# Kernel tuning notes

Measured on AMD Instinct MI355X. Metric: run time of the kernel, lower is better.

## Reference

```python
import jax, jax.numpy as jnp
import numpy as np

N = 300000   # total nodes
C = 32       # hidden states
M = 64       # discrete label alphabet
NGEN = 8     # number of generative models
G = 8192     # number of graphs


def setup_inputs() -> dict:
    key = jax.random.key(0)
    k1, k2, k3, k4 = jax.random.split(key, 4)
    B = jax.random.uniform(k1, (C, M, NGEN), minval=-5.0, maxval=5.0, dtype=jnp.float32)
    Pi = jax.random.uniform(k2, (C, NGEN), minval=-5.0, maxval=5.0, dtype=jnp.float32)
    x = jax.random.randint(k3, (N,), 0, M)
    batch = jnp.sort(jax.random.randint(k4, (N,), 0, G))
    return {"B": B, "Pi": Pi, "x": x, "batch": batch, "num_graphs": G}


def reference(B, Pi, x, batch, num_graphs):
    # softmax reparameterization: over M for B, over C for Pi (per generator)
    sm_B = jax.nn.softmax(B, axis=1)          # (C, M, n_gen)
    sm_Pi = jax.nn.softmax(Pi, axis=0)        # (C, n_gen)
    # gather per-node emission probs, then joint with prior -> (N, C, n_gen)
    numerator = sm_Pi[None, :, :] * jnp.transpose(sm_B[:, x, :], (1, 0, 2))
    posterior = numerator / numerator.sum(axis=1, keepdims=True)  # (N, C, n_gen)
    likelihood = (posterior * jnp.log(numerator)).sum(axis=1)     # (N, n_gen)
    # scatter-sum per graph
    likelihood = jax.ops.segment_sum(likelihood, batch, num_segments=num_graphs)  # (G, n_gen)
    h_vals = posterior.max(axis=1, keepdims=True)   # (N, 1, n_gen)
    h_idx = posterior.argmax(axis=1)                # (N, n_gen)
    return likelihood, h_vals, h_idx
```

## Files before the change

kernel.cpp:

```cpp
#include <hip/hip_runtime.h>

#define C_DIM 32
#define M_DIM 64
#define NG    8
#define TAB   (M_DIM * NG)
#define ST    9
#define SPB   1024


__global__ void __launch_bounds__(256)
cgmm_partials(const float* __restrict__ B, const float* __restrict__ Pi,
              const int* __restrict__ batch,
              float* __restrict__ Sexp, float* __restrict__ lsePi,
              int* __restrict__ starts, int N, int G) {
    const int tid = threadIdx.x;
    const int bid = blockIdx.x;

    if (bid < C_DIM) {
        __shared__ float row_s[M_DIM * NG];
        const float* row = B + bid * (M_DIM * NG);
        row_s[tid]       = row[tid];
        row_s[tid + 256] = row[tid + 256];
        __syncthreads();
        if (tid < NG) {
            float s = 0.f;
            #pragma unroll
            for (int m = 0; m < M_DIM; ++m) s += __expf(row_s[m * NG + tid]);
            Sexp[bid * NG + tid] = s;
        }
        return;
    }
    if (bid == C_DIM) {
        __shared__ float pi_s[C_DIM * NG];
        pi_s[tid] = Pi[tid];
        __syncthreads();
        if (tid < NG) {
            float s = 0.f;
            #pragma unroll
            for (int c = 0; c < C_DIM; ++c) s += __expf(pi_s[c * NG + tid]);
            lsePi[tid] = __logf(s);
        }
        return;
    }

    const int base = (bid - C_DIM - 1) * SPB;
    for (int i = tid; i < SPB; i += 256) {
        const int n = base + i;
        if (n >= N) break;
        const int bn = batch[n];
        if (n == 0) {
            for (int j = 0; j <= bn; ++j) starts[j] = 0;
        } else {
            const int bp = batch[n - 1];
            for (int j = bp + 1; j <= bn; ++j) starts[j] = n;
        }
        if (n == N - 1) {
            for (int j = bn + 1; j <= G; ++j) starts[j] = N;
        }
    }
}

__global__ void __launch_bounds__(512)
cgmm_tables(const float* __restrict__ B, const float* __restrict__ Pi,
            const float* __restrict__ Sexp, const float* __restrict__ lsePi,
            float* __restrict__ tab) {
    __shared__ float K_s[C_DIM * NG];
    const int tid = threadIdx.x;
    if (tid < C_DIM * NG)
        K_s[tid] = Pi[tid] - __logf(Sexp[tid]) - lsePi[tid & 7];
    __syncthreads();

    const int g = tid & 7;
    float L[C_DIM];
    float best = -1e30f; int bidx = 0;
    #pragma unroll
    for (int c = 0; c < C_DIM; ++c) {
        float v = B[c * (M_DIM * NG) + tid] + K_s[c * NG + g];
        L[c] = v;
        if (v > best) { best = v; bidx = c; }
    }
    float se = 0.f, la = 0.f;
    #pragma unroll
    for (int c = 0; c < C_DIM; ++c) {
        float e = __expf(L[c] - best);
        se += e; la += e * L[c];
    }
    tab[tid]           = la / se;
    tab[TAB + tid]     = 1.f / se;
    tab[2 * TAB + tid] = (float)bidx;
}

__global__ void __launch_bounds__(512)
cgmm_write(const int* __restrict__ x, const int* __restrict__ starts,
           const float* __restrict__ tab,
           float* __restrict__ out_like, float* __restrict__ out_hv,
           float* __restrict__ out_hi, int G) {
    __shared__ float like_s[M_DIM * ST];
    __shared__ float hval_s[M_DIM * ST];
    __shared__ float hidx_s[M_DIM * ST];
    const int tid = threadIdx.x;
    for (int i = tid; i < TAB; i += 512) {
        const int p = (i >> 3) * ST + (i & 7);
        like_s[p] = tab[i];
        hval_s[p] = tab[TAB + i];
        hidx_s[p] = tab[2 * TAB + i];
    }
    __syncthreads();

    const int j = blockIdx.x * 8 + (tid >> 6);
    if (j >= G) return;
    const int start = starts[j];
    const int end   = starts[j + 1];

    const int lane = tid & 63;
    const int slot = lane >> 3;
    const int g    = lane & 7;

    float4* hv4 = (float4*)out_hv;
    float4* hi4 = (float4*)out_hi;

    float acc = 0.f;
    for (int cb = start; cb < end; cb += 64) {
        const int cnt = end - cb;
        const int xv  = (cb + lane < end) ? x[cb + lane] : 0;

        #pragma unroll
        for (int s = 0; s < 2; ++s) {
            const int f    = s * 64 + lane;
            const int node = f >> 1;
            const int h    = (f & 1) * 4;
            const int xm   = __shfl(xv, node);
            if (node < cnt) {
                const int p = xm * ST + h;
                float4 v, w;
                v.x = hval_s[p];     v.y = hval_s[p + 1];
                v.z = hval_s[p + 2]; v.w = hval_s[p + 3];
                w.x = hidx_s[p];     w.y = hidx_s[p + 1];
                w.z = hidx_s[p + 2]; w.w = hidx_s[p + 3];
                hv4[(size_t)cb * 2 + f] = v;
                hi4[(size_t)cb * 2 + f] = w;
            }
        }
        #pragma unroll
        for (int t = 0; t < 8; ++t) {
            const int node = slot + 8 * t;
            const int xm   = __shfl(xv, node);
            if (node < cnt) acc += like_s[xm * ST + g];
        }
    }
    acc += __shfl_xor(acc, 8);
    acc += __shfl_xor(acc, 16);
    acc += __shfl_xor(acc, 32);
    if (lane < NG) out_like[(size_t)j * NG + g] = acc;
}

extern "C" void kernel_launch(void* const* d_in, const int* in_sizes, int n_in,
                              void* d_out, int out_size, void* d_ws, size_t ws_size,
                              hipStream_t stream) {
    const float* B     = (const float*)d_in[0];
    const float* Pi    = (const float*)d_in[1];
    const int*   x     = (const int*)d_in[2];
    const int*   batch = (const int*)d_in[3];
    const int N = in_sizes[2];
    const int G = (out_size - 2 * N * NG) / NG;

    float* tab    = (float*)d_ws;
    float* Sexp   = (float*)((char*)d_ws + 8192);
    float* lsePi  = (float*)((char*)d_ws + 9216);
    int*   starts = (int*)((char*)d_ws + 16384);

    float* out_like = (float*)d_out;
    float* out_hv   = out_like + (size_t)G * NG;
    float* out_hi   = out_hv + (size_t)N * NG;

    const int nsb = (N + SPB - 1) / SPB;

    cgmm_partials<<<C_DIM + 1 + nsb, 256, 0, stream>>>(B, Pi, batch, Sexp,
                                                       lsePi, starts, N, G);
    cgmm_tables<<<1, 512, 0, stream>>>(B, Pi, Sexp, lsePi, tab);
    cgmm_write<<<(G + 7) / 8, 512, 0, stream>>>(x, starts, tab, out_like,
                                                out_hv, out_hi, G);
}
```

Measured before the change: 19.74 us.

## Fuse softmax-normalizer and table kernels into the prep kernel

Merges the partials and table-building kernels into one prep kernel. Eight blocks each load all of B and Pi into padded shared memory, recompute the per-row normalizers and the prior log-sum-exp redundantly, then each builds the table entries for 8 labels. This removes one kernel launch and its serialization, plus the global round trip for Sexp and lsePi. The cost is redundant normalizer work in every table block and a 64KB shared-memory footprint per block.

```diff
diff --git a/kernel.cpp b/kernel.cpp
--- a/kernel.cpp
+++ b/kernel.cpp
@@ -5,45 +5,77 @@
 #define NG    8
 #define TAB   (M_DIM * NG)
 #define ST    9
+#define BST   520
 #define SPB   1024
+#define NTB   8
 
 
 __global__ void __launch_bounds__(256)
-cgmm_partials(const float* __restrict__ B, const float* __restrict__ Pi,
-              const int* __restrict__ batch,
-              float* __restrict__ Sexp, float* __restrict__ lsePi,
-              int* __restrict__ starts, int N, int G) {
+cgmm_prep(const float* __restrict__ B, const float* __restrict__ Pi,
+          const int* __restrict__ batch,
+          float* __restrict__ tab, int* __restrict__ starts,
+          int N, int G) {
     const int tid = threadIdx.x;
     const int bid = blockIdx.x;
 
-    if (bid < C_DIM) {
-        __shared__ float row_s[M_DIM * NG];
-        const float* row = B + bid * (M_DIM * NG);
-        row_s[tid]       = row[tid];
-        row_s[tid + 256] = row[tid + 256];
+    if (bid < NTB) {
+        __shared__ float Bs[C_DIM * BST];
+        __shared__ float Pis[C_DIM * NG];
+        __shared__ float lsePi_s[NG];
+        __shared__ float K_s[C_DIM * NG];
+
+        const float4* B4 = (const float4*)B;
+        float4* Bs4 = (float4*)Bs;
+        #pragma unroll
+        for (int i = tid; i < (C_DIM * M_DIM * NG) / 4; i += 256)
+            Bs4[(i >> 7) * (BST / 4) + (i & 127)] = B4[i];
+        if (tid < C_DIM * NG / 4) ((float4*)Pis)[tid] = ((const float4*)Pi)[tid];
         __syncthreads();
+
         if (tid < NG) {
             float s = 0.f;
             #pragma unroll
-            for (int m = 0; m < M_DIM; ++m) s += __expf(row_s[m * NG + tid]);
-            Sexp[bid * NG + tid] = s;
+            for (int c = 0; c < C_DIM; ++c) s += __expf(Pis[c * NG + tid]);
+            lsePi_s[tid] = __logf(s);
         }
-        return;
-    }
-    if (bid == C_DIM) {
-        __shared__ float pi_s[C_DIM * NG];
-        pi_s[tid] = Pi[tid];
         __syncthreads();
-        if (tid < NG) {
+
+        {
+            const int g = tid & 7;
+            const float* bp = Bs + (tid >> 3) * BST + g;
             float s = 0.f;
             #pragma unroll
-            for (int c = 0; c < C_DIM; ++c) s += __expf(pi_s[c * NG + tid]);
-            lsePi[tid] = __logf(s);
+            for (int m = 0; m < M_DIM; ++m) s += __expf(bp[m * NG]);
+            K_s[tid] = Pis[tid] - __logf(s) - lsePi_s[g];
+        }
+        __syncthreads();
+
+        if (tid < 64) {
+            const int m = bid * NTB + (tid >> 3);
+            const int g = tid & 7;
+            float L[C_DIM];
+            float best = -1e30f; int bidx = 0;
+            #pragma unroll
+            for (int c = 0; c < C_DIM; ++c) {
+                float v = Bs[c * BST + m * NG + g] + K_s[c * NG + g];
+                L[c] = v;
+                if (v > best) { best = v; bidx = c; }
+            }
+            float se = 0.f, la = 0.f;
+            #pragma unroll
+            for (int c = 0; c < C_DIM; ++c) {
+                float e = __expf(L[c] - best);
+                se += e; la += e * L[c];
+            }
+            const int idx = m * NG + g;
+            tab[idx]           = la / se;
+            tab[TAB + idx]     = 1.f / se;
+            tab[2 * TAB + idx] = (float)bidx;
         }
         return;
     }
 
-    const int base = (bid - C_DIM - 1) * SPB;
+    const int base = (bid - NTB) * SPB;
     for (int i = tid; i < SPB; i += 256) {
         const int n = base + i;
         if (n >= N) break;
@@ -58,36 +90,6 @@
             for (int j = bn + 1; j <= G; ++j) starts[j] = N;
         }
     }
-}
-
-__global__ void __launch_bounds__(512)
-cgmm_tables(const float* __restrict__ B, const float* __restrict__ Pi,
-            const float* __restrict__ Sexp, const float* __restrict__ lsePi,
-            float* __restrict__ tab) {
-    __shared__ float K_s[C_DIM * NG];
-    const int tid = threadIdx.x;
-    if (tid < C_DIM * NG)
-        K_s[tid] = Pi[tid] - __logf(Sexp[tid]) - lsePi[tid & 7];
-    __syncthreads();
-
-    const int g = tid & 7;
-    float L[C_DIM];
-    float best = -1e30f; int bidx = 0;
-    #pragma unroll
-    for (int c = 0; c < C_DIM; ++c) {
-        float v = B[c * (M_DIM * NG) + tid] + K_s[c * NG + g];
-        L[c] = v;
-        if (v > best) { best = v; bidx = c; }
-    }
-    float se = 0.f, la = 0.f;
-    #pragma unroll
-    for (int c = 0; c < C_DIM; ++c) {
-        float e = __expf(L[c] - best);
-        se += e; la += e * L[c];
-    }
-    tab[tid]           = la / se;
-    tab[TAB + tid]     = 1.f / se;
-    tab[2 * TAB + tid] = (float)bidx;
 }
 
 __global__ void __launch_bounds__(512)
@@ -165,8 +167,6 @@
     const int G = (out_size - 2 * N * NG) / NG;
 
     float* tab    = (float*)d_ws;
-    float* Sexp   = (float*)((char*)d_ws + 8192);
-    float* lsePi  = (float*)((char*)d_ws + 9216);
     int*   starts = (int*)((char*)d_ws + 16384);
 
     float* out_like = (float*)d_out;
@@ -175,9 +175,7 @@
 
     const int nsb = (N + SPB - 1) / SPB;
 
-    cgmm_partials<<<C_DIM + 1 + nsb, 256, 0, stream>>>(B, Pi, batch, Sexp,
-                                                       lsePi, starts, N, G);
-    cgmm_tables<<<1, 512, 0, stream>>>(B, Pi, Sexp, lsePi, tab);
+    cgmm_prep<<<NTB + nsb, 256, 0, stream>>>(B, Pi, batch, tab, starts, N, G);
     cgmm_write<<<(G + 7) / 8, 512, 0, stream>>>(x, starts, tab, out_like,
                                                 out_hv, out_hi, G);
 }
```

New measurement: 17.99 us. 1.1x faster.
